# Performance work log

Measured on AMD Instinct MI355X. Metric: run time of the kernel, lower is better.

Reference implementation:

```python
import jax, jax.numpy as jnp
import numpy as np

BS, DX, DY = 64, 512, 512


def setup_inputs() -> dict:
    key = jax.random.key(0)
    k1, k2, k3, k4, k5 = jax.random.split(key, 5)
    # ~1/3 of bins are zero -> ragged nonzero counts per sample
    hist = jax.random.randint(k1, (BS, DX, DY), 0, 3).astype(jnp.float32)
    xlo = jax.random.uniform(k2, (BS,)) * -5.0
    ylo = jax.random.uniform(k3, (BS,)) * -5.0
    x_lims = jnp.stack([xlo, xlo + 1.0 + 9.0 * jax.random.uniform(k4, (BS,))], axis=1)
    y_lims = jnp.stack([ylo, ylo + 1.0 + 9.0 * jax.random.uniform(k5, (BS,))], axis=1)
    return {"hist": hist, "x_lims": x_lims, "y_lims": y_lims}


def _grids(hist, x_lims, y_lims):
    bs, dx, dy = hist.shape
    cxw = (x_lims[:, 1] - x_lims[:, 0]) / dx  # [bs]
    cyw = (y_lims[:, 1] - y_lims[:, 0]) / dy
    cx = (jnp.linspace(0.0, 1.0, dx)[None, :] * cxw[:, None] * (dx - 1)
          + x_lims[:, 0:1] + cxw[:, None] / 2.0)  # [bs, dx]
    cy = (jnp.linspace(0.0, 1.0, dy)[None, :] * cyw[:, None] * (dy - 1)
          + y_lims[:, 0:1] + cyw[:, None] / 2.0)  # [bs, dy]
    hc = jnp.clip(hist, 0.0, 1.0)
    grid_x = cx[:, :, None] * hc  # [bs, dx, dy]
    grid_y = cy[:, None, :] * hc
    return grid_x, grid_y


def reference(hist, x_lims, y_lims):
    # as_sequence=True path. Data-dependent pad_sequence length is not
    # jit-able, so we pad to the full grid length L=dx*dy; the first lens[b]
    # entries per row match torch's ragged output, the rest are zeros
    # (torch's pad value). Stream compaction = stable argsort on the mask.
    bs, dx, dy = hist.shape
    L = dx * dy
    grid_x, grid_y = _grids(hist, x_lims, y_lims)
    mask = (hist != 0).reshape(bs, L)
    order = jnp.argsort(jnp.where(mask, 0, 1).astype(jnp.int32), axis=1, stable=True)
    pc_x = jnp.take_along_axis(grid_x.reshape(bs, L), order, axis=1)
    pc_y = jnp.take_along_axis(grid_y.reshape(bs, L), order, axis=1)
    pc_w = jnp.take_along_axis(hist.reshape(bs, L), order, axis=1)
    pc_w = jnp.where(jnp.take_along_axis(mask, order, axis=1), pc_w, 0.0)
    pc_lens = mask.sum(axis=1).astype(jnp.int32)  # [bs]
    return jnp.stack([pc_x, pc_y], axis=-1), pc_w, pc_lens
```

## Files before the change

kernel.cpp:

```cpp
#include <hip/hip_runtime.h>

#define BS 64
#define DX 512
#define DY 512
#define L (DX * DY)
#define TILE 4096
#define T_PER_S (L / TILE)
#define THREADS 256
#define EPT (TILE / THREADS)

typedef float vfloat2 __attribute__((ext_vector_type(2)));

__global__ __launch_bounds__(THREADS) void htpc_count(
    const float* __restrict__ hist, int* __restrict__ tile_count) {
  const int tile = blockIdx.x;
  const float4* h4 = (const float4*)(hist + (size_t)tile * TILE);

  int cnt = 0;
#pragma unroll
  for (int r = 0; r < EPT / 4; ++r) {
    float4 v = h4[r * THREADS + threadIdx.x];
    cnt += (v.x != 0.f) + (v.y != 0.f) + (v.z != 0.f) + (v.w != 0.f);
  }
  const int lane = threadIdx.x & 63;
  const int wv = threadIdx.x >> 6;
#pragma unroll
  for (int d = 32; d > 0; d >>= 1) cnt += __shfl_down(cnt, d);
  __shared__ int ws[THREADS / 64];
  if (lane == 0) ws[wv] = cnt;
  __syncthreads();
  if (threadIdx.x == 0) {
    int s = 0;
#pragma unroll
    for (int i = 0; i < THREADS / 64; ++i) s += ws[i];
    tile_count[tile] = s;
  }
}

__global__ __launch_bounds__(64) void htpc_scan(
    const int* __restrict__ tile_count, int* __restrict__ tile_off,
    float* __restrict__ out_lens, int* __restrict__ lens_i) {
  const int b = blockIdx.x;
  const int t = threadIdx.x;
  const int c = tile_count[b * T_PER_S + t];
  int incl = c;
#pragma unroll
  for (int d = 1; d < 64; d <<= 1) {
    int n = __shfl_up(incl, d);
    if (t >= d) incl += n;
  }
  tile_off[b * T_PER_S + t] = incl - c;
  if (t == 63) {
    out_lens[b] = (float)incl;
    lens_i[b] = incl;
  }
}

__global__ __launch_bounds__(THREADS) void htpc_compact_tail(
    const float* __restrict__ hist, const float* __restrict__ x_lims,
    const float* __restrict__ y_lims, const int* __restrict__ tile_off,
    const int* __restrict__ lens_i, float* __restrict__ out_pc,
    float* __restrict__ out_w) {
  __shared__ int sidx[TILE];
  __shared__ float sw[TILE];
  __shared__ int wsum[THREADS / 64];

  const int tile = blockIdx.x;
  const int b = tile / T_PER_S;
  const int t = tile % T_PER_S;
  const size_t gbase = (size_t)tile * TILE + (size_t)threadIdx.x * EPT;
  const float4* h4 = (const float4*)(hist + gbase);

  float v[EPT];
#pragma unroll
  for (int i = 0; i < EPT / 4; ++i) {
    float4 a = h4[i];
    v[i * 4 + 0] = a.x;
    v[i * 4 + 1] = a.y;
    v[i * 4 + 2] = a.z;
    v[i * 4 + 3] = a.w;
  }
  int cnt = 0;
#pragma unroll
  for (int i = 0; i < EPT; ++i) cnt += (v[i] != 0.f);

  const int lane = threadIdx.x & 63;
  const int wv = threadIdx.x >> 6;
  int incl = cnt;
#pragma unroll
  for (int d = 1; d < 64; d <<= 1) {
    int n = __shfl_up(incl, d);
    if (lane >= d) incl += n;
  }
  if (lane == 63) wsum[wv] = incl;
  __syncthreads();
  int wbase = 0, total = 0;
#pragma unroll
  for (int i = 0; i < THREADS / 64; ++i) {
    int s = wsum[i];
    if (i < wv) wbase += s;
    total += s;
  }
  int r = wbase + (incl - cnt);

  const int lidx0 = (int)(gbase - (size_t)b * L);
#pragma unroll
  for (int i = 0; i < EPT; ++i) {
    if (v[i] != 0.f) {
      sidx[r] = lidx0 + i;
      sw[r] = v[i];
      ++r;
    }
  }
  __syncthreads();

  const float xlo = x_lims[b * 2], xhi = x_lims[b * 2 + 1];
  const float ylo = y_lims[b * 2], yhi = y_lims[b * 2 + 1];
  const float cxw = (xhi - xlo) / DX;
  const float cyw = (yhi - ylo) / DY;

  const int off = tile_off[tile];
  vfloat2* pc2 = (vfloat2*)out_pc + (size_t)b * L;
  float* w = out_w + (size_t)b * L;

  for (int k = threadIdx.x; k < total; k += THREADS) {
    const int idx = sidx[k];
    const int ix = idx >> 9;
    const int iy = idx & 511;
    vfloat2 p;
    p.x = xlo + cxw * ((float)ix + 0.5f);
    p.y = ylo + cyw * ((float)iy + 0.5f);
    __builtin_nontemporal_store(p, pc2 + (off + k));
    __builtin_nontemporal_store(sw[k], w + (off + k));
  }

  const int len = lens_i[b];
  const int begin = t * TILE;
  const int end = begin + TILE;
  const int s0 = (len > begin) ? len : begin;
  const vfloat2 z = {0.f, 0.f};
  for (int i = s0 + (int)threadIdx.x; i < end; i += THREADS) {
    __builtin_nontemporal_store(z, pc2 + i);
    __builtin_nontemporal_store(0.f, w + i);
  }
}

extern "C" void kernel_launch(void* const* d_in, const int* in_sizes, int n_in,
                              void* d_out, int out_size, void* d_ws,
                              size_t ws_size, hipStream_t stream) {
  const float* hist = (const float*)d_in[0];
  const float* x_lims = (const float*)d_in[1];
  const float* y_lims = (const float*)d_in[2];

  float* out = (float*)d_out;
  float* out_pc = out;
  float* out_w = out + (size_t)BS * L * 2;
  float* out_lens = out_w + (size_t)BS * L;

  int* tile_count = (int*)d_ws;
  int* tile_off = tile_count + BS * T_PER_S;
  int* lens_i = tile_off + BS * T_PER_S;

  htpc_count<<<BS * T_PER_S, THREADS, 0, stream>>>(hist, tile_count);
  htpc_scan<<<BS, 64, 0, stream>>>(tile_count, tile_off, out_lens, lens_i);
  htpc_compact_tail<<<BS * T_PER_S, THREADS, 0, stream>>>(
      hist, x_lims, y_lims, tile_off, lens_i, out_pc, out_w);
}
```

Before: 264.7 us.

## Fuse per-sample tile scan into compaction kernel and vectorize zero-tail stores

Removes the separate scan kernel: each compaction block now recomputes the exclusive prefix over its sample's 64 tile counts in its first wavefront and keeps the offsets and total length in shared memory. This saves one kernel launch and the global round trip for the offsets. The zero-padding tail is also rewritten to use 16-byte vector nontemporal stores, with alignment peeling, instead of 8-byte and 4-byte stores. The cost is redundant scan work in every block, which is small.

```diff
diff --git a/kernel.cpp b/kernel.cpp
--- a/kernel.cpp
+++ b/kernel.cpp
@@ -10,6 +10,7 @@
 #define EPT (TILE / THREADS)
 
 typedef float vfloat2 __attribute__((ext_vector_type(2)));
+typedef float vfloat4 __attribute__((ext_vector_type(4)));
 
 __global__ __launch_bounds__(THREADS) void htpc_count(
     const float* __restrict__ hist, int* __restrict__ tile_count) {
@@ -37,37 +38,19 @@
   }
 }
 
-__global__ __launch_bounds__(64) void htpc_scan(
-    const int* __restrict__ tile_count, int* __restrict__ tile_off,
-    float* __restrict__ out_lens, int* __restrict__ lens_i) {
-  const int b = blockIdx.x;
-  const int t = threadIdx.x;
-  const int c = tile_count[b * T_PER_S + t];
-  int incl = c;
-#pragma unroll
-  for (int d = 1; d < 64; d <<= 1) {
-    int n = __shfl_up(incl, d);
-    if (t >= d) incl += n;
-  }
-  tile_off[b * T_PER_S + t] = incl - c;
-  if (t == 63) {
-    out_lens[b] = (float)incl;
-    lens_i[b] = incl;
-  }
-}
-
-__global__ __launch_bounds__(THREADS) void htpc_compact_tail(
+__global__ __launch_bounds__(THREADS) void htpc_fused(
     const float* __restrict__ hist, const float* __restrict__ x_lims,
-    const float* __restrict__ y_lims, const int* __restrict__ tile_off,
-    const int* __restrict__ lens_i, float* __restrict__ out_pc,
-    float* __restrict__ out_w) {
+    const float* __restrict__ y_lims, const int* __restrict__ tile_count,
+    float* __restrict__ out_pc, float* __restrict__ out_w,
+    float* __restrict__ out_lens) {
   __shared__ int sidx[TILE];
   __shared__ float sw[TILE];
+  __shared__ int s_off[T_PER_S + 1];
   __shared__ int wsum[THREADS / 64];
 
   const int tile = blockIdx.x;
-  const int b = tile / T_PER_S;
-  const int t = tile % T_PER_S;
+  const int b = tile >> 6;
+  const int t = tile & 63;
   const size_t gbase = (size_t)tile * TILE + (size_t)threadIdx.x * EPT;
   const float4* h4 = (const float4*)(hist + gbase);
 
@@ -80,6 +63,19 @@
     v[i * 4 + 2] = a.z;
     v[i * 4 + 3] = a.w;
   }
+
+  if (threadIdx.x < 64) {
+    const int c = tile_count[b * T_PER_S + threadIdx.x];
+    int incl = c;
+#pragma unroll
+    for (int d = 1; d < 64; d <<= 1) {
+      int n = __shfl_up(incl, d);
+      if ((int)threadIdx.x >= d) incl += n;
+    }
+    s_off[threadIdx.x] = incl - c;
+    if (threadIdx.x == 63) s_off[T_PER_S] = incl;
+  }
+
   int cnt = 0;
 #pragma unroll
   for (int i = 0; i < EPT; ++i) cnt += (v[i] != 0.f);
@@ -119,9 +115,12 @@
   const float cxw = (xhi - xlo) / DX;
   const float cyw = (yhi - ylo) / DY;
 
-  const int off = tile_off[tile];
+  const int off = s_off[t];
+  const int len = s_off[T_PER_S];
   vfloat2* pc2 = (vfloat2*)out_pc + (size_t)b * L;
   float* w = out_w + (size_t)b * L;
+
+  if (t == 0 && threadIdx.x == 0) out_lens[b] = (float)len;
 
   for (int k = threadIdx.x; k < total; k += THREADS) {
     const int idx = sidx[k];
@@ -134,14 +133,35 @@
     __builtin_nontemporal_store(sw[k], w + (off + k));
   }
 
-  const int len = lens_i[b];
   const int begin = t * TILE;
   const int end = begin + TILE;
-  const int s0 = (len > begin) ? len : begin;
-  const vfloat2 z = {0.f, 0.f};
-  for (int i = s0 + (int)threadIdx.x; i < end; i += THREADS) {
-    __builtin_nontemporal_store(z, pc2 + i);
-    __builtin_nontemporal_store(0.f, w + i);
+  int s0 = (len > begin) ? len : begin;
+  if (s0 < end) {
+    int a0 = s0;
+    if (a0 & 1) {
+      if (threadIdx.x == 0) {
+        const vfloat2 z2 = {0.f, 0.f};
+        __builtin_nontemporal_store(z2, pc2 + a0);
+      }
+      ++a0;
+    }
+    {
+      vfloat4* p4 = (vfloat4*)(pc2 + a0);
+      const int n4 = (end - a0) >> 1;
+      const vfloat4 z4 = {0.f, 0.f, 0.f, 0.f};
+      for (int k = threadIdx.x; k < n4; k += THREADS)
+        __builtin_nontemporal_store(z4, p4 + k);
+    }
+    const int head = (s0 + 3) & ~3;
+    if (threadIdx.x < (head - s0) && (s0 + (int)threadIdx.x) < end)
+      __builtin_nontemporal_store(0.f, w + s0 + threadIdx.x);
+    if (head < end) {
+      vfloat4* w4 = (vfloat4*)(w + head);
+      const int n4 = (end - head) >> 2;
+      const vfloat4 z4 = {0.f, 0.f, 0.f, 0.f};
+      for (int k = threadIdx.x; k < n4; k += THREADS)
+        __builtin_nontemporal_store(z4, w4 + k);
+    }
   }
 }
 
@@ -158,11 +178,8 @@
   float* out_lens = out_w + (size_t)BS * L;
 
   int* tile_count = (int*)d_ws;
-  int* tile_off = tile_count + BS * T_PER_S;
-  int* lens_i = tile_off + BS * T_PER_S;
 
   htpc_count<<<BS * T_PER_S, THREADS, 0, stream>>>(hist, tile_count);
-  htpc_scan<<<BS, 64, 0, stream>>>(tile_count, tile_off, out_lens, lens_i);
-  htpc_compact_tail<<<BS * T_PER_S, THREADS, 0, stream>>>(
-      hist, x_lims, y_lims, tile_off, lens_i, out_pc, out_w);
+  htpc_fused<<<BS * T_PER_S, THREADS, 0, stream>>>(
+      hist, x_lims, y_lims, tile_count, out_pc, out_w, out_lens);
 }
```

After: 262.3 us. About the same (-0.9%).
